# Kernel optimization log

Hardware: AMD Instinct MI355X
Metric: run time of the kernel (lower is better)

The kernel has to match this reference:

```python
import jax, jax.numpy as jnp
from jax import lax
import numpy as np

EMBED = 20
FILTERS = 16
KSIZES = (1, 3, 5, 7, 9)
LIN_IN = 7 * len(KSIZES) * FILTERS  # 560
LIN_DIM = 64
SEQ_LENS = {'pep': 12, 'a1': 7, 'a2': 8, 'a3': 16, 'b1': 6, 'b2': 7, 'b3': 18}
BATCH = 16384


def setup_inputs() -> dict:
    key = jax.random.key(0)
    keys = jax.random.split(key, 16)
    inp = {}
    for i, (name, L) in enumerate(SEQ_LENS.items()):
        inp[name] = jax.random.normal(keys[i], (BATCH, EMBED, L), dtype=jnp.float32)
    # Conv weights: one stacked array per kernel size, [7 sequences, FILTERS, EMBED, k]
    for j, k in enumerate(KSIZES):
        inp[f'Wk{k}'] = jax.random.normal(keys[7 + j], (7, FILTERS, EMBED, k), dtype=jnp.float32) * 0.1
    inp['lin1_w'] = jax.random.normal(keys[12], (LIN_DIM, LIN_IN), dtype=jnp.float32) * 0.05
    inp['lin1_b'] = jnp.zeros((LIN_DIM,), dtype=jnp.float32)
    inp['lin2_w'] = jax.random.normal(keys[13], (1, LIN_DIM), dtype=jnp.float32) * 0.1
    inp['lin2_b'] = jnp.zeros((1,), dtype=jnp.float32)
    return inp


def _conv_relu_gmax(x, w):
    # x: [B, C, L], w: [F, C, k] -> SAME conv + ReLU + global max over length -> [B, F]
    y = lax.conv_general_dilated(x, w, window_strides=(1,), padding='SAME',
                                 dimension_numbers=('NCH', 'OIH', 'NCH'))
    return jnp.max(jax.nn.relu(y), axis=-1)


def _branch(x, ws):
    # x scaled by 1/5 as in the torch forward; concat pooled features over kernel sizes
    x = x / 5.0
    return jnp.concatenate([_conv_relu_gmax(x, w) for w in ws], axis=1)  # [B, 5*F]


def reference(pep, a1, a2, a3, b1, b2, b3, Wk1, Wk3, Wk5, Wk7, Wk9,
              lin1_w, lin1_b, lin2_w, lin2_b):
    seqs = [pep, a1, a2, a3, b1, b2, b3]
    Wks = [Wk1, Wk3, Wk5, Wk7, Wk9]
    feats = jnp.concatenate(
        [_branch(seqs[i], [W[i] for W in Wks]) for i in range(7)], axis=1)  # [B, 560]
    # Dropout is identity at inference.
    h = jax.nn.sigmoid(feats @ lin1_w.T + lin1_b)  # [B, 64]
    out = h @ lin2_w.T + lin2_b                    # [B, 1]
    return out.reshape(-1)                          # [B]
```

## Files before the change

kernel.cpp:

```cpp
#include <hip/hip_runtime.h>
#include <stdint.h>
#include <stddef.h>

typedef short bfrag __attribute__((ext_vector_type(8)));
typedef float f32x4 __attribute__((ext_vector_type(4)));

#define NSEQ 7

__constant__ int c_ks[5] = {1, 3, 5, 7, 9};

#define SLO0 3
#define SLO1 2
#define SLO2 1
#define SLO3 0
#define SLO4 0
#define SN0 1
#define SN1 3
#define SN2 5
#define SN3 6
#define SN4 7

static __device__ __forceinline__ unsigned short f2bf(float f) {
  unsigned int u = __float_as_uint(f);
  u += 0x7FFFu + ((u >> 16) & 1u);
  return (unsigned short)(u >> 16);
}

struct PrepArgs {
  const float* Wk[5];
  const float* lin1_w;
  bfrag* Wpack;
  bfrag* lin1pack;
};

__global__ __launch_bounds__(256) void prep_kernel(PrepArgs a) {
  int tid = blockIdx.x * 256 + threadIdx.x;
  const int NW = NSEQ * 5 * 7 * 64;
  if (tid < NW) {
    int lane = tid & 63, rest = tid >> 6;
    int step = rest % 7, nt = (rest / 7) % 5, seq = rest / 35;
    int quad = lane >> 4, f = lane & 15;
    int ks = c_ks[nt], off = (9 - ks) >> 1;
    const float* W = a.Wk[nt];
    bfrag s;
#pragma unroll
    for (int j = 0; j < 8; ++j) {
      int k = step * 32 + quad * 8 + j;
      int t = k / 24, c = k % 24;
      int tap = t - off;
      float val = 0.f;
      if (c < 20 && tap >= 0 && tap < ks)
        val = W[((seq * 16 + f) * 20 + c) * ks + tap] * 0.2f;
      s[j] = (short)f2bf(val);
    }
    a.Wpack[tid] = s;
  } else if (tid < NW + 4 * 18 * 64) {
    int t2 = tid - NW;
    int lane = t2 & 63, rest = t2 >> 6;
    int step = rest % 18, nt = rest / 18;
    int quad = lane >> 4, col = lane & 15;
    int n = nt * 16 + col;
    bfrag s;
#pragma unroll
    for (int j = 0; j < 8; ++j) {
      int k = step * 32 + quad * 8 + j;
      float val = (k < 560) ? a.lin1_w[n * 560 + k] : 0.f;
      s[j] = (short)f2bf(val);
    }
    a.lin1pack[t2] = s;
  }
}

struct ConvArgs {
  const float* x[NSEQ];
  const bfrag* Wpack;
  unsigned short* feats;
};

static __device__ __forceinline__ void store_feat(unsigned short* feats, int b, int k, float v) {
  int step = k >> 5, q = (k >> 3) & 3, j = k & 7;
  feats[((size_t)(b >> 4) * 18 + step) * 512 + (q * 16 + (b & 15)) * 8 + j] = f2bf(v);
}

template <int Lc, int SHIFTc, int MTc, int TBBv, int Pv>
__device__ __forceinline__ void conv_body(unsigned short* xl, const ConvArgs& a,
                                          const int seq, const int b0) {
  const int tid = threadIdx.x;
  const float* xg = a.x[seq];

  for (int i = tid; i < TBBv * Pv * 24 / 8; i += 256) ((uint4*)xl)[i] = uint4{0, 0, 0, 0};
  __syncthreads();
  for (int r = tid; r < TBBv * 20; r += 256) {
    int b = r / 20, c = r % 20;
    const float* src = xg + (size_t)((b0 + b) * 20 + c) * Lc;
    unsigned short* dst = xl + (b * Pv + 4) * 24 + c;
#pragma unroll
    for (int xi = 0; xi < Lc; ++xi) dst[xi * 24] = f2bf(src[xi]);
  }
  __syncthreads();

  const int wave = tid >> 6, lane = tid & 63, quad = lane >> 4, m = lane & 15;

  const bfrag* wp = a.Wpack + (size_t)(seq * 5 * 7) * 64 + lane;
  bfrag Bf[22];
  {
    int bi = 0;
#pragma unroll
    for (int i = 0; i < SN0; ++i) Bf[bi++] = wp[(0 * 7 + SLO0 + i) * 64];
#pragma unroll
    for (int i = 0; i < SN1; ++i) Bf[bi++] = wp[(1 * 7 + SLO1 + i) * 64];
#pragma unroll
    for (int i = 0; i < SN2; ++i) Bf[bi++] = wp[(2 * 7 + SLO2 + i) * 64];
#pragma unroll
    for (int i = 0; i < SN3; ++i) Bf[bi++] = wp[(3 * 7 + SLO3 + i) * 64];
#pragma unroll
    for (int i = 0; i < SN4; ++i) Bf[bi++] = wp[(4 * 7 + SLO4 + i) * 64];
  }

  constexpr int njobs = (MTc == 2) ? TBBv : ((TBBv << SHIFTc) >> 4);
  constexpr int bpt = (MTc == 1 && SHIFTc == 3) ? 2 : 1;
  constexpr int lmask = (1 << SHIFTc) - 1;

  for (int job = wave; job < njobs; job += 4) {
    float v0 = 0.f, v1 = 0.f, v2 = 0.f, v3 = 0.f, v4 = 0.f;
#pragma unroll
    for (int sub = 0; sub < MTc; ++sub) {
      int bl, l;
      if (MTc == 2) { bl = job; l = sub * 2 + m; }
      else { int r = job * 16 + m; bl = r >> SHIFTc; l = r & lmask; }
      const unsigned short* arow = &xl[(bl * Pv + l) * 24 + quad * 8];
      f32x4 acc0 = {0.f, 0.f, 0.f, 0.f}, acc1 = acc0, acc2 = acc0, acc3 = acc0, acc4 = acc0;
#pragma unroll
      for (int s = 0; s < 7; ++s) {
        bfrag Af = *(const bfrag*)(arow + s * 32);
        if (s >= SLO0 && s < SLO0 + SN0)
          acc0 = __builtin_amdgcn_mfma_f32_16x16x32_bf16(Af, Bf[0 + s - SLO0], acc0, 0, 0, 0);
        if (s >= SLO1 && s < SLO1 + SN1)
          acc1 = __builtin_amdgcn_mfma_f32_16x16x32_bf16(Af, Bf[1 + s - SLO1], acc1, 0, 0, 0);
        if (s >= SLO2 && s < SLO2 + SN2)
          acc2 = __builtin_amdgcn_mfma_f32_16x16x32_bf16(Af, Bf[4 + s - SLO2], acc2, 0, 0, 0);
        if (s >= SLO3 && s < SLO3 + SN3)
          acc3 = __builtin_amdgcn_mfma_f32_16x16x32_bf16(Af, Bf[9 + s - SLO3], acc3, 0, 0, 0);
        acc4 = __builtin_amdgcn_mfma_f32_16x16x32_bf16(Af, Bf[15 + s], acc4, 0, 0, 0);
      }
#pragma unroll
      for (int r4 = 0; r4 < 4; ++r4) {
        bool ok = (MTc == 2) ? true : (((quad * 4 + r4) & lmask) < Lc);
        v0 = fmaxf(v0, ok ? acc0[r4] : 0.f);
        v1 = fmaxf(v1, ok ? acc1[r4] : 0.f);
        v2 = fmaxf(v2, ok ? acc2[r4] : 0.f);
        v3 = fmaxf(v3, ok ? acc3[r4] : 0.f);
        v4 = fmaxf(v4, ok ? acc4[r4] : 0.f);
      }
    }
    v0 = fmaxf(v0, __shfl_xor(v0, 16));
    v1 = fmaxf(v1, __shfl_xor(v1, 16));
    v2 = fmaxf(v2, __shfl_xor(v2, 16));
    v3 = fmaxf(v3, __shfl_xor(v3, 16));
    v4 = fmaxf(v4, __shfl_xor(v4, 16));
    if (bpt == 1) {
      v0 = fmaxf(v0, __shfl_xor(v0, 32));
      v1 = fmaxf(v1, __shfl_xor(v1, 32));
      v2 = fmaxf(v2, __shfl_xor(v2, 32));
      v3 = fmaxf(v3, __shfl_xor(v3, 32));
      v4 = fmaxf(v4, __shfl_xor(v4, 32));
      if (lane < 16) {
        int b = b0 + job, kb = seq * 80 + lane;
        store_feat(a.feats, b, kb, v0);      store_feat(a.feats, b, kb + 16, v1);
        store_feat(a.feats, b, kb + 32, v2); store_feat(a.feats, b, kb + 48, v3);
        store_feat(a.feats, b, kb + 64, v4);
      }
    } else {
      if ((lane & 16) == 0) {
        int b = b0 + job * 2 + (lane >> 5), kb = seq * 80 + (lane & 15);
        store_feat(a.feats, b, kb, v0);      store_feat(a.feats, b, kb + 16, v1);
        store_feat(a.feats, b, kb + 32, v2); store_feat(a.feats, b, kb + 48, v3);
        store_feat(a.feats, b, kb + 64, v4);
      }
    }
  }
}

__global__ __launch_bounds__(256, 3) void conv_kernel(ConvArgs a) {
  __shared__ __align__(16) unsigned short xl[32 * 25 * 24];
  const int bid = blockIdx.x;
  if (bid < 3072) {
    const int seq = bid >> 9, b0 = (bid & 511) * 32;
    switch (seq) {
      case 0: conv_body<12, 4, 1, 32, 25>(xl, a, 0, b0); break;
      case 1: conv_body< 7, 3, 1, 32, 25>(xl, a, 1, b0); break;
      case 2: conv_body< 8, 3, 1, 32, 25>(xl, a, 2, b0); break;
      case 3: conv_body<16, 4, 1, 32, 25>(xl, a, 3, b0); break;
      case 4: conv_body< 6, 3, 1, 32, 25>(xl, a, 4, b0); break;
      default: conv_body< 7, 3, 1, 32, 25>(xl, a, 5, b0); break;
    }
  } else {
    conv_body<18, 5, 2, 16, 41>(xl, a, 6, (bid - 3072) * 16);
  }
}

struct MlpArgs {
  const bfrag* feats;
  const bfrag* lin1pack;
  const float* lin1_b;
  const float* lin2_w;
  const float* lin2_b;
  float* out;
};

__global__ __launch_bounds__(256, 4) void mlp_kernel(MlpArgs a) {
  __shared__ float h[32 * 68];
  __shared__ float w2[64];
  const int tid = threadIdx.x;
  const int b0 = blockIdx.x * 32, bt0 = b0 >> 4;
  if (tid < 64) w2[tid] = a.lin2_w[tid];
  const int wave = tid >> 6, lane = tid & 63, quad = lane >> 4, m = lane & 15;
  const int nt = wave;
  bfrag Bf[18];
#pragma unroll
  for (int s = 0; s < 18; ++s) Bf[s] = a.lin1pack[(nt * 18 + s) * 64 + lane];
  int n = nt * 16 + m;
  float bias = a.lin1_b[n];
#pragma unroll
  for (int bt = 0; bt < 2; ++bt) {
    const bfrag* ap = a.feats + (size_t)(bt0 + bt) * 18 * 64 + lane;
    f32x4 acc = {0.f, 0.f, 0.f, 0.f};
#pragma unroll
    for (int s = 0; s < 18; ++s)
      acc = __builtin_amdgcn_mfma_f32_16x16x32_bf16(ap[s * 64], Bf[s], acc, 0, 0, 0);
#pragma unroll
    for (int r = 0; r < 4; ++r) {
      float pre = acc[r] + bias;
      h[(bt * 16 + quad * 4 + r) * 68 + n] = 1.f / (1.f + __expf(-pre));
    }
  }
  __syncthreads();
  int bl = tid >> 3, q = tid & 7;
  const float* hr = &h[bl * 68 + q * 8];
  float s = 0.f;
#pragma unroll
  for (int j = 0; j < 8; ++j) s += hr[j] * w2[q * 8 + j];
  s += __shfl_xor(s, 1);
  s += __shfl_xor(s, 2);
  s += __shfl_xor(s, 4);
  if (q == 0) a.out[b0 + bl] = s + a.lin2_b[0];
}

extern "C" void kernel_launch(void* const* d_in, const int* in_sizes, int n_in,
                              void* d_out, int out_size, void* d_ws, size_t ws_size,
                              hipStream_t stream) {
  (void)in_sizes; (void)n_in; (void)out_size; (void)ws_size;
  char* ws = (char*)d_ws;
  bfrag* Wpack = (bfrag*)(ws + 0);
  bfrag* lin1pack = (bfrag*)(ws + 262144);
  unsigned short* feats = (unsigned short*)(ws + 393216);

  PrepArgs pa;
  for (int j = 0; j < 5; ++j) pa.Wk[j] = (const float*)d_in[7 + j];
  pa.lin1_w = (const float*)d_in[12];
  pa.Wpack = Wpack;
  pa.lin1pack = lin1pack;
  prep_kernel<<<80, 256, 0, stream>>>(pa);

  ConvArgs ca;
  for (int i = 0; i < NSEQ; ++i) ca.x[i] = (const float*)d_in[i];
  ca.Wpack = Wpack;
  ca.feats = feats;
  conv_kernel<<<4096, 256, 0, stream>>>(ca);

  MlpArgs ma;
  ma.feats = (const bfrag*)feats;
  ma.lin1pack = lin1pack;
  ma.lin1_b = (const float*)d_in[13];
  ma.lin2_w = (const float*)d_in[14];
  ma.lin2_b = (const float*)d_in[15];
  ma.out = (float*)d_out;
  mlp_kernel<<<16384 / 32, 256, 0, stream>>>(ma);
}
```

Baseline: 183.3 us.

## Vectorize conv input staging, raise conv occupancy, halve MLP block batch

The conv input staging now reads the contiguous batch slab with float4 loads and scatters the bf16-converted elements into the transposed LDS layout, replacing per-thread strided scalar loads. The conv kernel's launch bound goes from 3 to 4 blocks per CU, which may force register spills given the 22 held B fragments. The MLP kernel now processes 16 rows per block over 1024 blocks instead of 32 rows over 512, for more parallelism at the cost of reloading lin1 weights twice as often. The index divisions in the new staging loop add ALU work in exchange for coalesced global reads.

```diff
diff --git a/kernel.cpp b/kernel.cpp
--- a/kernel.cpp
+++ b/kernel.cpp
@@ -90,12 +90,20 @@
 
   for (int i = tid; i < TBBv * Pv * 24 / 8; i += 256) ((uint4*)xl)[i] = uint4{0, 0, 0, 0};
   __syncthreads();
-  for (int r = tid; r < TBBv * 20; r += 256) {
-    int b = r / 20, c = r % 20;
-    const float* src = xg + (size_t)((b0 + b) * 20 + c) * Lc;
-    unsigned short* dst = xl + (b * Pv + 4) * 24 + c;
-#pragma unroll
-    for (int xi = 0; xi < Lc; ++xi) dst[xi * 24] = f2bf(src[xi]);
+  {
+    constexpr int NF4 = TBBv * 20 * Lc / 4;
+    const float* xb = xg + (size_t)b0 * 20 * Lc;
+    for (int i4 = tid; i4 < NF4; i4 += 256) {
+      float4 v = *(const float4*)(xb + i4 * 4);
+#pragma unroll
+      for (int e = 0; e < 4; ++e) {
+        int flat = i4 * 4 + e;
+        int b = flat / (20 * Lc), rem = flat % (20 * Lc);
+        int c = rem / Lc, xi = rem % Lc;
+        float val = (e == 0) ? v.x : (e == 1) ? v.y : (e == 2) ? v.z : v.w;
+        xl[(b * Pv + 4 + xi) * 24 + c] = f2bf(val);
+      }
+    }
   }
   __syncthreads();
 
@@ -181,7 +189,7 @@
   }
 }
 
-__global__ __launch_bounds__(256, 3) void conv_kernel(ConvArgs a) {
+__global__ __launch_bounds__(256, 4) void conv_kernel(ConvArgs a) {
   __shared__ __align__(16) unsigned short xl[32 * 25 * 24];
   const int bid = blockIdx.x;
   if (bid < 3072) {
@@ -209,40 +217,36 @@
 };
 
 __global__ __launch_bounds__(256, 4) void mlp_kernel(MlpArgs a) {
-  __shared__ float h[32 * 68];
+  __shared__ float h[16 * 68];
   __shared__ float w2[64];
   const int tid = threadIdx.x;
-  const int b0 = blockIdx.x * 32, bt0 = b0 >> 4;
+  const int b0 = blockIdx.x * 16;
   if (tid < 64) w2[tid] = a.lin2_w[tid];
   const int wave = tid >> 6, lane = tid & 63, quad = lane >> 4, m = lane & 15;
   const int nt = wave;
   bfrag Bf[18];
 #pragma unroll
   for (int s = 0; s < 18; ++s) Bf[s] = a.lin1pack[(nt * 18 + s) * 64 + lane];
+  const bfrag* ap = a.feats + (size_t)blockIdx.x * 18 * 64 + lane;
+  f32x4 acc = {0.f, 0.f, 0.f, 0.f};
+#pragma unroll
+  for (int s = 0; s < 18; ++s)
+    acc = __builtin_amdgcn_mfma_f32_16x16x32_bf16(ap[s * 64], Bf[s], acc, 0, 0, 0);
   int n = nt * 16 + m;
   float bias = a.lin1_b[n];
 #pragma unroll
-  for (int bt = 0; bt < 2; ++bt) {
-    const bfrag* ap = a.feats + (size_t)(bt0 + bt) * 18 * 64 + lane;
-    f32x4 acc = {0.f, 0.f, 0.f, 0.f};
-#pragma unroll
-    for (int s = 0; s < 18; ++s)
-      acc = __builtin_amdgcn_mfma_f32_16x16x32_bf16(ap[s * 64], Bf[s], acc, 0, 0, 0);
-#pragma unroll
-    for (int r = 0; r < 4; ++r) {
-      float pre = acc[r] + bias;
-      h[(bt * 16 + quad * 4 + r) * 68 + n] = 1.f / (1.f + __expf(-pre));
-    }
+  for (int r = 0; r < 4; ++r) {
+    float pre = acc[r] + bias;
+    h[(quad * 4 + r) * 68 + n] = 1.f / (1.f + __expf(-pre));
   }
   __syncthreads();
-  int bl = tid >> 3, q = tid & 7;
-  const float* hr = &h[bl * 68 + q * 8];
-  float s = 0.f;
-#pragma unroll
-  for (int j = 0; j < 8; ++j) s += hr[j] * w2[q * 8 + j];
+  int bl = tid >> 4, q = tid & 15;
+  const float* hr = &h[bl * 68 + q * 4];
+  float s = hr[0] * w2[q * 4] + hr[1] * w2[q * 4 + 1] + hr[2] * w2[q * 4 + 2] + hr[3] * w2[q * 4 + 3];
   s += __shfl_xor(s, 1);
   s += __shfl_xor(s, 2);
   s += __shfl_xor(s, 4);
+  s += __shfl_xor(s, 8);
   if (q == 0) a.out[b0 + bl] = s + a.lin2_b[0];
 }
 
@@ -275,5 +279,5 @@
   ma.lin2_w = (const float*)d_in[14];
   ma.lin2_b = (const float*)d_in[15];
   ma.out = (float*)d_out;
-  mlp_kernel<<<16384 / 32, 256, 0, stream>>>(ma);
-}
+  mlp_kernel<<<1024, 256, 0, stream>>>(ma);
+}
```

New measurement: 188.3 us. 2.7% more time.
